# Kernel optimization log

Measured on AMD Instinct MI355X. Metric: run time of the kernel, lower is better.

The kernel has to match this reference:

```python
import jax, jax.numpy as jnp
import numpy as np

B, S, D, H, L, DFF = 32, 512, 1024, 16, 4, 2048
DK = D // H
NEG = -1e32
EPS = 1e-5


def setup_inputs() -> dict:
    key = jax.random.key(0)
    ks = jax.random.split(key, 8)
    std = 0.02
    inp = {
        "q_embed": jax.random.normal(ks[0], (B, S, D), jnp.float32),
        "qa_embed": jax.random.normal(ks[1], (B, S, D), jnp.float32),
        # per-block stacked params [L, ...]; torch Linear stored as [in, out]
        "Wk": jax.random.normal(ks[2], (L, D, D), jnp.float32) * std,
        "bk": jnp.zeros((L, D), jnp.float32),
        "Wv": jax.random.normal(ks[3], (L, D, D), jnp.float32) * std,
        "bv": jnp.zeros((L, D), jnp.float32),
        "Wo": jax.random.normal(ks[4], (L, D, D), jnp.float32) * std,
        "bo": jnp.zeros((L, D), jnp.float32),
        "ln1_s": jnp.ones((L, D), jnp.float32),
        "ln1_b": jnp.zeros((L, D), jnp.float32),
        "W1": jax.random.normal(ks[5], (L, D, DFF), jnp.float32) * std,
        "b1": jnp.zeros((L, DFF), jnp.float32),
        "W2": jax.random.normal(ks[6], (L, DFF, D), jnp.float32) * std,
        "b2": jnp.zeros((L, D), jnp.float32),
        "ln2_s": jnp.ones((L, D), jnp.float32),
        "ln2_b": jnp.zeros((L, D), jnp.float32),
    }
    return inp


def _ln(x, s, b):
    m = jnp.mean(x, axis=-1, keepdims=True)
    v = jnp.mean((x - m) ** 2, axis=-1, keepdims=True)
    return (x - m) / jnp.sqrt(v + EPS) * s + b


def _block(x, y, Wk, bk, Wv, bv, Wo, bo, l1s, l1b, W1, b1, W2, b2, l2s, l2b, allowed):
    # kq_same=1: q and k both use k_linear; q == k since query == key == x
    qk = (x @ Wk + bk).reshape(B, S, H, DK).transpose(0, 2, 1, 3)  # [B,H,S,DK]
    v = (y @ Wv + bv).reshape(B, S, H, DK).transpose(0, 2, 1, 3)
    scores = jnp.einsum("bhid,bhjd->bhij", qk, qk) / np.sqrt(DK)
    scores = jnp.where(allowed, scores, NEG)  # strictly-causal mask
    attn = jax.nn.softmax(scores, axis=-1)
    attn = attn * (jnp.arange(S)[None, None, :, None] > 0)  # zero_pad row 0
    o = jnp.einsum("bhij,bhjd->bhid", attn, v)  # [B,H,S,DK]
    o = o.transpose(0, 2, 1, 3).reshape(B, S, D) @ Wo + bo
    x = _ln(x + o, l1s, l1b)
    f = jax.nn.relu(x @ W1 + b1) @ W2 + b2
    return _ln(x + f, l2s, l2b)


def reference(q_embed, qa_embed, Wk, bk, Wv, bv, Wo, bo, ln1_s, ln1_b,
              W1, b1, W2, b2, ln2_s, ln2_b):
    allowed = jnp.tril(jnp.ones((S, S), bool), -1)  # j < i
    x, y = q_embed, qa_embed
    for i in range(L):
        x = _block(x, y, Wk[i], bk[i], Wv[i], bv[i], Wo[i], bo[i],
                   ln1_s[i], ln1_b[i], W1[i], b1[i], W2[i], b2[i],
                   ln2_s[i], ln2_b[i], allowed)
    return x
```

## Files before the change

kernel.cpp:

```cpp
#include <hip/hip_runtime.h>

#define B_ 32
#define S_ 512
#define D_ 1024
#define H_ 16
#define DK_ 64
#define DFF_ 2048
#define L_ 4

typedef __attribute__((ext_vector_type(8))) short short8;
typedef __attribute__((ext_vector_type(4))) float f32x4;
typedef unsigned short u16;
typedef unsigned int u32;
typedef __attribute__((ext_vector_type(4))) u16 u16x4;
typedef __attribute__((ext_vector_type(8))) u16 u16x8;

__device__ __forceinline__ u16 f2bf(float f) {
    u32 u = __float_as_uint(f);
    u = u + 0x7fffu + ((u >> 16) & 1u);
    return (u16)(u >> 16);
}
__device__ __forceinline__ u16 f2bf_t(float f) {
    return (u16)(__float_as_uint(f) >> 16);
}
__device__ __forceinline__ float bf2f(u16 v) {
    return __uint_as_float(((u32)v) << 16);
}

__device__ __forceinline__ void async16(const u16* g, u16* l) {
    __builtin_amdgcn_global_load_lds((const __attribute__((address_space(1))) u32*)g,
                                     (__attribute__((address_space(3))) u32*)l, 16, 0, 0);
}

#define LGKM0_FENCE                                                            \
    asm volatile("s_waitcnt lgkmcnt(0)" ::: "memory");                         \
    __builtin_amdgcn_sched_barrier(0);

#define MFQ(MQ, NQ, BQ)                                                        \
    __builtin_amdgcn_s_setprio(1);                                             \
    _Pragma("unroll")                                                          \
    for (int r = 0; r < 4; r++) {                                              \
        _Pragma("unroll")                                                      \
        for (int c = 0; c < 2; c++) {                                          \
            _Pragma("unroll")                                                  \
            for (int kf = 0; kf < 2; kf++)                                     \
                acc[(MQ)*4+r][(NQ)*2+c] =                                      \
                    __builtin_amdgcn_mfma_f32_16x16x32_bf16(                   \
                        a[r][kf], BQ[c][kf], acc[(MQ)*4+r][(NQ)*2+c], 0,0,0);  \
        }                                                                      \
    }                                                                          \
    __builtin_amdgcn_s_setprio(0);

#define RD_AQ(CBA, MQ)                                                         \
    _Pragma("unroll")                                                          \
    for (int r = 0; r < 4; r++) {                                              \
        a[r][0] = *(const short8*)&lds[(CBA) + arow + (MQ)*4096 + r*1024 + chv0]; \
        a[r][1] = *(const short8*)&lds[(CBA) + arow + (MQ)*4096 + r*1024 + chv1]; \
    }

#define RD_BQ(DST, CBB, NQ)                                                    \
    _Pragma("unroll")                                                          \
    for (int c = 0; c < 2; c++) {                                              \
        DST[c][0] = *(const short8*)&lds[(CBB) + brow + (NQ)*2048 + c*1024 + chv0]; \
        DST[c][1] = *(const short8*)&lds[(CBB) + brow + (NQ)*2048 + c*1024 + chv1]; \
    }

template<int RELU, int OUTM>
__global__ __launch_bounds__(512, 2)
void gemm256(const u16* __restrict__ A, const u16* __restrict__ Bt,
             const float* __restrict__ bias, void* __restrict__ C,
             int M, int N, int K)
{
    __shared__ __align__(16) u16 lds[65536];
    const int t = threadIdx.x;
    const int w = t >> 6, l = t & 63;
    const int lane16 = l & 15, quad = l >> 4;
    const int wm = w >> 2, wn = w & 3;

    const int gx = gridDim.x;
    const int nwg = gx * gridDim.y;
    const int orig = blockIdx.y * gx + blockIdx.x;
    const int q8 = nwg >> 3, r8 = nwg & 7;
    const int xcd = orig & 7, sidx = orig >> 3;
    const int nid = (xcd < r8 ? xcd * (q8 + 1) : r8 * (q8 + 1) + (xcd - r8) * q8) + sidx;
    const int m0 = (nid / gx) * 256;
    const int n0 = (nid % gx) * 256;

    f32x4 acc[8][4];
#pragma unroll
    for (int i = 0; i < 8; i++)
#pragma unroll
        for (int j = 0; j < 4; j++) acc[i][j] = f32x4{0.f, 0.f, 0.f, 0.f};

    const int lr = l >> 3;
    const int xorcol = ((l & 7) ^ lr) * 8;
    const int aw8 = (w < 4 ? w * 8 : 128 + (w - 4) * 8);
    const u16* Asrc = A + (size_t)(m0 + aw8 + lr) * K + xorcol;
    const u16* Bsrc = Bt + (size_t)(n0 + w * 8 + lr) * K + xorcol;

    auto stageA = [&](int tile, int q) {
        const int c = tile & 1;
        async16(Asrc + (size_t)(q * 32) * K + (tile << 6),
                &lds[c * 16384 + (aw8 + q * 32) * 64]);
    };
    auto stageB = [&](int tile, int j) {
        const int c = tile & 1;
        async16(Bsrc + (size_t)(j * 64) * K + (tile << 6),
                &lds[32768 + c * 16384 + (j * 64 + w * 8) * 64]);
    };

    const int chv0 = ((0 + quad) ^ (lane16 & 7)) * 8;
    const int chv1 = ((4 + quad) ^ (lane16 & 7)) * 8;
    const int arow = (wm * 128 + lane16) * 64;
    const int brow = (wn * 64 + lane16) * 64;

    const int NT = K >> 6;
    const int niter = NT >> 1;

    stageA(0, 0); stageA(0, 1); stageA(0, 2); stageA(0, 3);
    stageB(0, 0); stageB(0, 1); stageB(0, 2); stageB(0, 3);
    stageA(1, 0); stageA(1, 1);
    stageB(1, 0); stageB(1, 1); stageB(1, 2); stageB(1, 3);
    stageA(1, 2); stageA(1, 3);
    asm volatile("s_waitcnt vmcnt(8)" ::: "memory");
    __builtin_amdgcn_sched_barrier(0);
    __builtin_amdgcn_s_barrier();

    short8 a[4][2], b0[2][2], b1[2][2];

    for (int it = 0; it < niter; it++) {
        const bool hn = (it + 1 < niter);
        const int e2 = 2 * it + 2, o2 = 2 * it + 3;

        RD_AQ(0, 0)
        RD_BQ(b0, 32768, 0)
        asm volatile("s_waitcnt lgkmcnt(8)" ::: "memory");
        __builtin_amdgcn_s_barrier();
        LGKM0_FENCE
        MFQ(0, 0, b0)
        __builtin_amdgcn_s_barrier();
        RD_BQ(b1, 32768, 1)
        if (hn) { stageA(e2, 0); stageA(e2, 1); }
        __builtin_amdgcn_s_barrier();
        LGKM0_FENCE
        MFQ(0, 1, b1)
        __builtin_amdgcn_s_barrier();
        RD_AQ(0, 1)
        if (hn) { stageB(e2, 0); stageB(e2, 1); }
        __builtin_amdgcn_s_barrier();
        LGKM0_FENCE
        MFQ(1, 0, b0)
        __builtin_amdgcn_s_barrier();
        if (hn) { stageB(e2, 2); stageB(e2, 3); stageA(e2, 2); stageA(e2, 3); }
        __builtin_amdgcn_s_barrier();
        MFQ(1, 1, b1)
        if (hn) asm volatile("s_waitcnt vmcnt(8)" ::: "memory");
        else    asm volatile("s_waitcnt vmcnt(0)" ::: "memory");
        __builtin_amdgcn_sched_barrier(0);
        __builtin_amdgcn_s_barrier();

        RD_AQ(16384, 0)
        RD_BQ(b0, 49152, 0)
        asm volatile("s_waitcnt lgkmcnt(8)" ::: "memory");
        __builtin_amdgcn_s_barrier();
        LGKM0_FENCE
        MFQ(0, 0, b0)
        __builtin_amdgcn_s_barrier();
        RD_BQ(b1, 49152, 1)
        if (hn) { stageA(o2, 0); stageA(o2, 1); }
        __builtin_amdgcn_s_barrier();
        LGKM0_FENCE
        MFQ(0, 1, b1)
        __builtin_amdgcn_s_barrier();
        RD_AQ(16384, 1)
        if (hn) { stageB(o2, 0); stageB(o2, 1); }
        __builtin_amdgcn_s_barrier();
        LGKM0_FENCE
        MFQ(1, 0, b0)
        __builtin_amdgcn_s_barrier();
        if (hn) { stageB(o2, 2); stageB(o2, 3); stageA(o2, 2); stageA(o2, 3); }
        __builtin_amdgcn_s_barrier();
        MFQ(1, 1, b1)
        if (hn) asm volatile("s_waitcnt vmcnt(8)" ::: "memory");
        __builtin_amdgcn_sched_barrier(0);
        __builtin_amdgcn_s_barrier();
    }

#pragma unroll
    for (int mi = 0; mi < 8; mi++) {
#pragma unroll
        for (int ni = 0; ni < 4; ni++) {
            int col = n0 + wn * 64 + ni * 16 + lane16;
            float bv = bias[col];
            if (OUTM == 2) {
                int tok0 = m0 + wm * 128 + mi * 16 + quad * 4;
                int bb = tok0 >> 9, s0 = tok0 & 511;
                int hh = col >> 6, dd = col & 63;
                u16x4 pk;
#pragma unroll
                for (int r2 = 0; r2 < 4; r2++) pk[r2] = f2bf(acc[mi][ni][r2] + bv);
                *(u16x4*)&((u16*)C)[(((size_t)bb * H_ + hh) * DK_ + dd) * S_ + s0] = pk;
            } else {
                int row = m0 + wm * 128 + mi * 16 + quad * 4;
#pragma unroll
                for (int r2 = 0; r2 < 4; r2++) {
                    float v = acc[mi][ni][r2] + bv;
                    if (RELU) v = fmaxf(v, 0.f);
                    size_t idx = (size_t)(row + r2) * N + col;
                    if (OUTM == 1) ((u16*)C)[idx] = f2bf(v);
                    else           ((float*)C)[idx] = v;
                }
            }
        }
    }
}

__global__ __launch_bounds__(256, 3)
void attn_kernel(const u16* __restrict__ qk, const u16* __restrict__ vt,
                 u16* __restrict__ ao)
{
    __shared__ __align__(16) u16 sP[4][32 * 72];
    const int t = threadIdx.x, w = t >> 6, l = t & 63;
    const int lane16 = l & 15, quad = l >> 4;
    const int p = blockIdx.x;
    const int bh = blockIdx.y;
    const int b = bh >> 4, h = bh & 15;
    const int band = (w < 2) ? (2 * p + w) : (15 - 2 * p - (w - 2));
    const int band0 = band * 32;
    const u16* kb = qk + (size_t)b * S_ * D_ + h * DK_;
    const u16* vb = vt + (size_t)bh * DK_ * S_;
    u16* aob = ao + (size_t)b * S_ * D_ + h * DK_;
    const float SC = 0.125f * 1.44269504f;
    u16* myP = sP[w];

    short8 bq[2][2];
#pragma unroll
    for (int ii = 0; ii < 2; ii++)
#pragma unroll
        for (int kf = 0; kf < 2; kf++)
            bq[ii][kf] = *(const short8*)(kb + (size_t)(band0 + ii * 16 + lane16) * D_ +
                                          kf * 32 + quad * 8);

    f32x4 aco[4][2];
    float lsum[2] = {0.f, 0.f};
#pragma unroll
    for (int di = 0; di < 4; di++)
#pragma unroll
        for (int ii = 0; ii < 2; ii++) aco[di][ii] = f32x4{0.f, 0.f, 0.f, 0.f};

    const int ntiles = (band >> 1) + 1;
    for (int jt = 0; jt < ntiles; jt++) {
        const int j0 = jt * 64;
        const bool diag = (jt == ntiles - 1);

        short8 aK[2][4];
#pragma unroll
        for (int kf = 0; kf < 2; kf++)
#pragma unroll
            for (int ji = 0; ji < 4; ji++)
                aK[kf][ji] = *(const short8*)(kb + (size_t)(j0 + ji * 16 + lane16) * D_ +
                                              kf * 32 + quad * 8);
        f32x4 sacc[4][2];
#pragma unroll
        for (int ji = 0; ji < 4; ji++)
#pragma unroll
            for (int ii = 0; ii < 2; ii++) sacc[ji][ii] = f32x4{0.f, 0.f, 0.f, 0.f};
#pragma unroll
        for (int kf = 0; kf < 2; kf++)
#pragma unroll
            for (int ji = 0; ji < 4; ji++)
#pragma unroll
                for (int ii = 0; ii < 2; ii++)
                    sacc[ji][ii] = __builtin_amdgcn_mfma_f32_16x16x32_bf16(
                        aK[kf][ji], bq[ii][kf], sacc[ji][ii], 0, 0, 0);

        short8 aV[2][4];
#pragma unroll
        for (int kf = 0; kf < 2; kf++)
#pragma unroll
            for (int di = 0; di < 4; di++)
                aV[kf][di] = *(const short8*)(vb + (size_t)(di * 16 + lane16) * S_ +
                                              j0 + kf * 32 + quad * 8);

#pragma unroll
        for (int ii = 0; ii < 2; ii++) {
#pragma unroll
            for (int ji = 0; ji < 4; ji++) {
                u16x4 pk;
#pragma unroll
                for (int r2 = 0; r2 < 4; r2++) {
                    float v = sacc[ji][ii][r2] * SC;
                    if (diag) {
                        int j = j0 + ji * 16 + quad * 4 + r2;
                        int i = band0 + ii * 16 + lane16;
                        if (j >= i) v = -3e38f;
                    }
                    float pv = exp2f(v);
                    lsum[ii] += pv;
                    pk[r2] = f2bf_t(pv);
                }
                *(u16x4*)&myP[(ii * 16 + lane16) * 72 + ji * 16 + quad * 4] = pk;
            }
        }

        short8 pf[2][2];
#pragma unroll
        for (int kf = 0; kf < 2; kf++)
#pragma unroll
            for (int ii = 0; ii < 2; ii++)
                pf[kf][ii] = *(const short8*)&myP[(ii * 16 + lane16) * 72 +
                                                  kf * 32 + quad * 8];
#pragma unroll
        for (int kf = 0; kf < 2; kf++)
#pragma unroll
            for (int di = 0; di < 4; di++)
#pragma unroll
                for (int ii = 0; ii < 2; ii++)
                    aco[di][ii] = __builtin_amdgcn_mfma_f32_16x16x32_bf16(
                        aV[kf][di], pf[kf][ii], aco[di][ii], 0, 0, 0);
    }

#pragma unroll
    for (int ii = 0; ii < 2; ii++) {
        lsum[ii] += __shfl_xor(lsum[ii], 16);
        lsum[ii] += __shfl_xor(lsum[ii], 32);
    }

#pragma unroll
    for (int ii = 0; ii < 2; ii++) {
        int row = band0 + ii * 16 + lane16;
        float lv = lsum[ii];
        float inv = (row == 0 || !(lv > 0.f)) ? 0.f : 1.f / lv;
#pragma unroll
        for (int di = 0; di < 4; di++) {
            u16x4 o;
#pragma unroll
            for (int r2 = 0; r2 < 4; r2++) o[r2] = f2bf(aco[di][ii][r2] * inv);
            *(u16x4*)&aob[(size_t)row * D_ + di * 16 + quad * 4] = o;
        }
    }
}

template<int XBF, int WF32>
__global__ __launch_bounds__(256)
void ln_kernel(const void* __restrict__ xin, const float* __restrict__ addv,
               const float* __restrict__ sc, const float* __restrict__ bi,
               u16* __restrict__ xb_out, float* __restrict__ f32_out)
{
    const int row = blockIdx.x;
    const int t = threadIdx.x;
    const int w = t >> 6, l = t & 63;
    __shared__ float red[8];
    f32x4 a;
    if (XBF) {
        u16x4 raw = ((const u16x4*)xin)[(size_t)row * 256 + t];
#pragma unroll
        for (int j = 0; j < 4; j++) a[j] = bf2f(raw[j]);
    } else {
        a = ((const f32x4*)xin)[(size_t)row * 256 + t];
    }
    f32x4 c = ((const f32x4*)(addv + (size_t)row * D_))[t];
    f32x4 v;
    float s1 = 0.f, s2 = 0.f;
#pragma unroll
    for (int j = 0; j < 4; j++) {
        v[j] = a[j] + c[j];
        s1 += v[j];
        s2 += v[j] * v[j];
    }
#pragma unroll
    for (int off = 32; off > 0; off >>= 1) {
        s1 += __shfl_xor(s1, off);
        s2 += __shfl_xor(s2, off);
    }
    if (l == 0) { red[w * 2] = s1; red[w * 2 + 1] = s2; }
    __syncthreads();
    s1 = red[0] + red[2] + red[4] + red[6];
    s2 = red[1] + red[3] + red[5] + red[7];
    float mean = s1 * (1.f / D_);
    float var = s2 * (1.f / D_) - mean * mean;
    float rstd = rsqrtf(var + 1e-5f);
    f32x4 s4 = ((const f32x4*)sc)[t];
    f32x4 b4 = ((const f32x4*)bi)[t];
    f32x4 o;
    u16x4 ob;
#pragma unroll
    for (int j = 0; j < 4; j++) {
        o[j] = (v[j] - mean) * rstd * s4[j] + b4[j];
        ob[j] = f2bf(o[j]);
    }
    ((u16x4*)(xb_out + (size_t)row * D_))[t] = ob;
    if (WF32) ((f32x4*)(f32_out + (size_t)row * D_))[t] = o;
}

__global__ void cvt_kernel(const float* __restrict__ in, u16* __restrict__ out, int n4)
{
    int i = blockIdx.x * blockDim.x + threadIdx.x;
    if (i < n4) {
        f32x4 v = ((const f32x4*)in)[i];
        u16x4 o;
#pragma unroll
        for (int j = 0; j < 4; j++) o[j] = f2bf(v[j]);
        ((u16x4*)out)[i] = o;
    }
}

__device__ __forceinline__ void tconv_body(const float* W, u16* WT, int K, int N,
                                           int bx, int by, int t)
{
    __shared__ float tile[64][65];
    const int n0 = bx * 64, k0 = by * 64;
#pragma unroll
    for (int i = 0; i < 4; i++) {
        int kr = (t >> 4) + i * 16;
        int nc = (t & 15) * 4;
        f32x4 v = *(const f32x4*)&W[(size_t)(k0 + kr) * N + n0 + nc];
        tile[kr][nc] = v[0]; tile[kr][nc + 1] = v[1];
        tile[kr][nc + 2] = v[2]; tile[kr][nc + 3] = v[3];
    }
    __syncthreads();
#pragma unroll
    for (int i = 0; i < 4; i++) {
        int nr = (t >> 4) + i * 16;
        int kc = (t & 15) * 4;
        u16x4 o;
#pragma unroll
        for (int j = 0; j < 4; j++) o[j] = f2bf(tile[kc + j][nr]);
        *(u16x4*)&WT[(size_t)(n0 + nr) * K + k0 + kc] = o;
    }
}

__global__ __launch_bounds__(256)
void wconv_kernel(const float* __restrict__ Wk, const float* __restrict__ Wv,
                  const float* __restrict__ Wo, const float* __restrict__ W1f,
                  const float* __restrict__ W2f,
                  u16* __restrict__ wk, u16* __restrict__ wv, u16* __restrict__ wo,
                  u16* __restrict__ w1, u16* __restrict__ w2)
{
    const int idx = blockIdx.x;
    const float* W; u16* T; int K, N, bx, by;
    if (idx < 768) {
        int wsel = idx >> 8, t16 = idx & 255;
        W = (wsel == 0) ? Wk : (wsel == 1) ? Wv : Wo;
        T = (wsel == 0) ? wk : (wsel == 1) ? wv : wo;
        K = 1024; N = 1024; bx = t16 & 15; by = t16 >> 4;
    } else if (idx < 1280) {
        int i = idx - 768;
        W = W1f; T = w1; K = 1024; N = 2048; bx = i & 31; by = i >> 5;
    } else {
        int i = idx - 1280;
        W = W2f; T = w2; K = 2048; N = 1024; bx = i & 15; by = i >> 4;
    }
    tconv_body(W, T, K, N, bx, by, threadIdx.x);
}

extern "C" void kernel_launch(void* const* d_in, const int* in_sizes, int n_in,
                              void* d_out, int out_size, void* d_ws, size_t ws_size,
                              hipStream_t stream)
{
    const float* q_embed = (const float*)d_in[0];
    const float* qa_embed = (const float*)d_in[1];
    const float* Wk = (const float*)d_in[2];
    const float* bk = (const float*)d_in[3];
    const float* Wv = (const float*)d_in[4];
    const float* bv = (const float*)d_in[5];
    const float* Wo = (const float*)d_in[6];
    const float* bo = (const float*)d_in[7];
    const float* ln1_s = (const float*)d_in[8];
    const float* ln1_b = (const float*)d_in[9];
    const float* W1 = (const float*)d_in[10];
    const float* b1 = (const float*)d_in[11];
    const float* W2 = (const float*)d_in[12];
    const float* b2 = (const float*)d_in[13];
    const float* ln2_s = (const float*)d_in[14];
    const float* ln2_b = (const float*)d_in[15];
    (void)in_sizes; (void)n_in; (void)out_size;

    char* ws = (char*)d_ws;
    size_t off = 0;
    auto carve = [&](size_t bytes) -> char* {
        char* p = ws + off;
        off += (bytes + 255) & ~(size_t)255;
        return p;
    };
    const size_t NTOK = (size_t)B_ * S_;
    u16* wk = (u16*)carve((size_t)D_ * D_ * 2);
    u16* wv = (u16*)carve((size_t)D_ * D_ * 2);
    u16* wo = (u16*)carve((size_t)D_ * D_ * 2);
    u16* w1 = (u16*)carve((size_t)D_ * DFF_ * 2);
    u16* w2 = (u16*)carve((size_t)DFF_ * D_ * 2);
    u16* x = (u16*)carve(NTOK * D_ * 2);
    u16* U12 = (u16*)carve(NTOK * DFF_ * 2);
    u16* U3 = (u16*)carve(NTOK * D_ * 2);
    size_t off_overlay = off;
    u16* ybf_sep = (u16*)carve(NTOK * D_ * 2);
    bool sep = (ws_size >= off);
    if (!sep) off = off_overlay;
    if (ws_size < off) return;

    u16* qkb = U12;
    u16* vbf = U12 + NTOK * D_;
    u16* hb = U12;
    u16* aob = U3;
    u16* ybf = sep ? ybf_sep : U3;
    float* of32 = (float*)d_out;

    cvt_kernel<<<16384, 256, 0, stream>>>(q_embed, x, (int)(NTOK * D_ / 4));
    if (sep)
        cvt_kernel<<<16384, 256, 0, stream>>>(qa_embed, ybf, (int)(NTOK * D_ / 4));

    const dim3 G1024(4, 64), G2048(8, 64);
    for (int lyr = 0; lyr < L_; lyr++) {
        const size_t wsq = (size_t)lyr * D_ * D_;
        const size_t wf1 = (size_t)lyr * D_ * DFF_;
        wconv_kernel<<<1792, 256, 0, stream>>>(Wk + wsq, Wv + wsq, Wo + wsq,
                                               W1 + wf1, W2 + wf1,
                                               wk, wv, wo, w1, w2);
        if (!sep)
            cvt_kernel<<<16384, 256, 0, stream>>>(qa_embed, ybf, (int)(NTOK * D_ / 4));
        gemm256<0, 1><<<G1024, 512, 0, stream>>>(x, wk, bk + lyr * D_,
                                                 qkb, (int)NTOK, D_, D_);
        gemm256<0, 2><<<G1024, 512, 0, stream>>>(ybf, wv, bv + lyr * D_,
                                                 vbf, (int)NTOK, D_, D_);
        attn_kernel<<<dim3(4, B_ * H_), 256, 0, stream>>>(qkb, vbf, aob);
        gemm256<0, 0><<<G1024, 512, 0, stream>>>(aob, wo, bo + lyr * D_,
                                                 of32, (int)NTOK, D_, D_);
        if (lyr == 0)
            ln_kernel<0, 0><<<(int)NTOK, 256, 0, stream>>>(q_embed, of32,
                ln1_s + lyr * D_, ln1_b + lyr * D_, x, nullptr);
        else
            ln_kernel<1, 0><<<(int)NTOK, 256, 0, stream>>>(x, of32,
                ln1_s + lyr * D_, ln1_b + lyr * D_, x, nullptr);
        gemm256<1, 1><<<G2048, 512, 0, stream>>>(x, w1, b1 + lyr * DFF_,
                                                 hb, (int)NTOK, DFF_, D_);
        gemm256<0, 0><<<G1024, 512, 0, stream>>>(hb, w2, b2 + lyr * D_,
                                                 of32, (int)NTOK, D_, DFF_);
        if (lyr == L_ - 1)
            ln_kernel<1, 1><<<(int)NTOK, 256, 0, stream>>>(x, of32,
                ln2_s + lyr * D_, ln2_b + lyr * D_, x, (float*)d_out);
        else
            ln_kernel<1, 0><<<(int)NTOK, 256, 0, stream>>>(x, of32,
                ln2_s + lyr * D_, ln2_b + lyr * D_, x, nullptr);
    }
}
```

Before: 1.759 ms.

## Double-buffer K tile loads in attention and remap block indices for locality

The attention loop is unrolled by two with ping-pong K register buffers, so the next tile's K fragments are loaded while the current tile's softmax and PV MFMAs run. The grid becomes 1D with a swizzled block-to-(band, head) mapping that places the four band-pair blocks of nearby heads close together in launch order, aiming for better cache reuse. Launch bounds drop from 3 to 2 waves-per-EU to make room for the extra registers, which lowers possible occupancy.

```diff
diff --git a/kernel.cpp b/kernel.cpp
--- a/kernel.cpp
+++ b/kernel.cpp
@@ -215,15 +215,87 @@
     }
 }
 
-__global__ __launch_bounds__(256, 3)
+#define ATT_TILE(KC, KN)                                                       \
+    {                                                                          \
+        const int j0 = jt * 64;                                                \
+        const bool diag = (jt == ntiles - 1);                                  \
+        f32x4 sacc[4][2];                                                      \
+        _Pragma("unroll")                                                      \
+        for (int ji = 0; ji < 4; ji++)                                         \
+            _Pragma("unroll")                                                  \
+            for (int ii = 0; ii < 2; ii++)                                     \
+                sacc[ji][ii] = f32x4{0.f, 0.f, 0.f, 0.f};                      \
+        _Pragma("unroll")                                                      \
+        for (int kf = 0; kf < 2; kf++)                                         \
+            _Pragma("unroll")                                                  \
+            for (int ji = 0; ji < 4; ji++)                                     \
+                _Pragma("unroll")                                              \
+                for (int ii = 0; ii < 2; ii++)                                 \
+                    sacc[ji][ii] = __builtin_amdgcn_mfma_f32_16x16x32_bf16(    \
+                        KC[kf][ji], bq[ii][kf], sacc[ji][ii], 0, 0, 0);        \
+        short8 aV[2][4];                                                       \
+        _Pragma("unroll")                                                      \
+        for (int kf = 0; kf < 2; kf++)                                         \
+            _Pragma("unroll")                                                  \
+            for (int di = 0; di < 4; di++)                                     \
+                aV[kf][di] = *(const short8*)(vb +                             \
+                    (size_t)(di * 16 + lane16) * S_ + j0 + kf * 32 + quad * 8);\
+        if (!diag) {                                                           \
+            _Pragma("unroll")                                                  \
+            for (int kf = 0; kf < 2; kf++)                                     \
+                _Pragma("unroll")                                              \
+                for (int ji = 0; ji < 4; ji++)                                 \
+                    KN[kf][ji] = *(const short8*)(kb +                         \
+                        (size_t)(j0 + 64 + ji * 16 + lane16) * D_ +            \
+                        kf * 32 + quad * 8);                                   \
+        }                                                                      \
+        _Pragma("unroll")                                                      \
+        for (int ii = 0; ii < 2; ii++) {                                       \
+            _Pragma("unroll")                                                  \
+            for (int ji = 0; ji < 4; ji++) {                                   \
+                u16x4 pk;                                                      \
+                _Pragma("unroll")                                              \
+                for (int r2 = 0; r2 < 4; r2++) {                               \
+                    float v = sacc[ji][ii][r2] * SC;                           \
+                    if (diag) {                                                \
+                        int j = j0 + ji * 16 + quad * 4 + r2;                  \
+                        int i = band0 + ii * 16 + lane16;                      \
+                        if (j >= i) v = -3e38f;                                \
+                    }                                                          \
+                    float pv = exp2f(v);                                       \
+                    lsum[ii] += pv;                                            \
+                    pk[r2] = f2bf_t(pv);                                       \
+                }                                                              \
+                *(u16x4*)&myP[(ii * 16 + lane16) * 72 + ji * 16 + quad * 4] = pk; \
+            }                                                                  \
+        }                                                                      \
+        short8 pf[2][2];                                                       \
+        _Pragma("unroll")                                                      \
+        for (int kf = 0; kf < 2; kf++)                                         \
+            _Pragma("unroll")                                                  \
+            for (int ii = 0; ii < 2; ii++)                                     \
+                pf[kf][ii] = *(const short8*)&myP[(ii * 16 + lane16) * 72 +    \
+                                                  kf * 32 + quad * 8];         \
+        _Pragma("unroll")                                                      \
+        for (int kf = 0; kf < 2; kf++)                                         \
+            _Pragma("unroll")                                                  \
+            for (int di = 0; di < 4; di++)                                     \
+                _Pragma("unroll")                                              \
+                for (int ii = 0; ii < 2; ii++)                                 \
+                    aco[di][ii] = __builtin_amdgcn_mfma_f32_16x16x32_bf16(     \
+                        aV[kf][di], pf[kf][ii], aco[di][ii], 0, 0, 0);         \
+    }
+
+__global__ __launch_bounds__(256, 2)
 void attn_kernel(const u16* __restrict__ qk, const u16* __restrict__ vt,
                  u16* __restrict__ ao)
 {
     __shared__ __align__(16) u16 sP[4][32 * 72];
     const int t = threadIdx.x, w = t >> 6, l = t & 63;
     const int lane16 = l & 15, quad = l >> 4;
-    const int p = blockIdx.x;
-    const int bh = blockIdx.y;
+    const int bid = blockIdx.x;
+    const int p = (bid >> 3) & 3;
+    const int bh = (bid & 7) | ((bid >> 5) << 3);
     const int b = bh >> 4, h = bh & 15;
     const int band = (w < 2) ? (2 * p + w) : (15 - 2 * p - (w - 2));
     const int band0 = band * 32;
@@ -249,75 +321,21 @@
         for (int ii = 0; ii < 2; ii++) aco[di][ii] = f32x4{0.f, 0.f, 0.f, 0.f};
 
     const int ntiles = (band >> 1) + 1;
-    for (int jt = 0; jt < ntiles; jt++) {
-        const int j0 = jt * 64;
-        const bool diag = (jt == ntiles - 1);
-
-        short8 aK[2][4];
-#pragma unroll
-        for (int kf = 0; kf < 2; kf++)
-#pragma unroll
-            for (int ji = 0; ji < 4; ji++)
-                aK[kf][ji] = *(const short8*)(kb + (size_t)(j0 + ji * 16 + lane16) * D_ +
-                                              kf * 32 + quad * 8);
-        f32x4 sacc[4][2];
+
+    short8 aKa[2][4], aKb[2][4];
+#pragma unroll
+    for (int kf = 0; kf < 2; kf++)
 #pragma unroll
         for (int ji = 0; ji < 4; ji++)
-#pragma unroll
-            for (int ii = 0; ii < 2; ii++) sacc[ji][ii] = f32x4{0.f, 0.f, 0.f, 0.f};
-#pragma unroll
-        for (int kf = 0; kf < 2; kf++)
-#pragma unroll
-            for (int ji = 0; ji < 4; ji++)
-#pragma unroll
-                for (int ii = 0; ii < 2; ii++)
-                    sacc[ji][ii] = __builtin_amdgcn_mfma_f32_16x16x32_bf16(
-                        aK[kf][ji], bq[ii][kf], sacc[ji][ii], 0, 0, 0);
-
-        short8 aV[2][4];
-#pragma unroll
-        for (int kf = 0; kf < 2; kf++)
-#pragma unroll
-            for (int di = 0; di < 4; di++)
-                aV[kf][di] = *(const short8*)(vb + (size_t)(di * 16 + lane16) * S_ +
-                                              j0 + kf * 32 + quad * 8);
-
-#pragma unroll
-        for (int ii = 0; ii < 2; ii++) {
-#pragma unroll
-            for (int ji = 0; ji < 4; ji++) {
-                u16x4 pk;
-#pragma unroll
-                for (int r2 = 0; r2 < 4; r2++) {
-                    float v = sacc[ji][ii][r2] * SC;
-                    if (diag) {
-                        int j = j0 + ji * 16 + quad * 4 + r2;
-                        int i = band0 + ii * 16 + lane16;
-                        if (j >= i) v = -3e38f;
-                    }
-                    float pv = exp2f(v);
-                    lsum[ii] += pv;
-                    pk[r2] = f2bf_t(pv);
-                }
-                *(u16x4*)&myP[(ii * 16 + lane16) * 72 + ji * 16 + quad * 4] = pk;
-            }
-        }
-
-        short8 pf[2][2];
-#pragma unroll
-        for (int kf = 0; kf < 2; kf++)
-#pragma unroll
-            for (int ii = 0; ii < 2; ii++)
-                pf[kf][ii] = *(const short8*)&myP[(ii * 16 + lane16) * 72 +
-                                                  kf * 32 + quad * 8];
-#pragma unroll
-        for (int kf = 0; kf < 2; kf++)
-#pragma unroll
-            for (int di = 0; di < 4; di++)
-#pragma unroll
-                for (int ii = 0; ii < 2; ii++)
-                    aco[di][ii] = __builtin_amdgcn_mfma_f32_16x16x32_bf16(
-                        aV[kf][di], pf[kf][ii], aco[di][ii], 0, 0, 0);
+            aKa[kf][ji] = *(const short8*)(kb + (size_t)(ji * 16 + lane16) * D_ +
+                                           kf * 32 + quad * 8);
+
+    int jt = 0;
+    for (;;) {
+        ATT_TILE(aKa, aKb)
+        if (++jt >= ntiles) break;
+        ATT_TILE(aKb, aKa)
+        if (++jt >= ntiles) break;
     }
 
 #pragma unroll
@@ -522,7 +540,7 @@
                                                  qkb, (int)NTOK, D_, D_);
         gemm256<0, 2><<<G1024, 512, 0, stream>>>(ybf, wv, bv + lyr * D_,
                                                  vbf, (int)NTOK, D_, D_);
-        attn_kernel<<<dim3(4, B_ * H_), 256, 0, stream>>>(qkb, vbf, aob);
+        attn_kernel<<<2048, 256, 0, stream>>>(qkb, vbf, aob);
         gemm256<0, 0><<<G1024, 512, 0, stream>>>(aob, wo, bo + lyr * D_,
                                                  of32, (int)NTOK, D_, D_);
         if (lyr == 0)
```

New measurement: 1.755 ms. Within noise of the previous version (-0.2%).
